# Performance work log

Hardware: AMD Instinct MI355X
Metric: run time of the kernel (lower is better)

The kernel has to match this reference:

```python
import math
import jax, jax.numpy as jnp
import numpy as np

B, S, D = 2, 2048, 1024
H = 8
HD = D // H // 2            # 64, per-branch head dim
ROT = HD // 2               # 32, rotary rot_dim (RotaryEmbedding dim=head_dim//2)
DEPTH = 2
LAMBDA_INIT = 0.8 - 0.6 * math.exp(-0.3 * DEPTH)


def rope(t):
    # t: (b, s, heads, HD); rotate first ROT dims with interleaved pairs
    s = t.shape[1]
    inv = 1.0 / (10000.0 ** (jnp.arange(0, ROT, 2, dtype=jnp.float32) / ROT))  # (ROT/2,)
    freqs = jnp.arange(s, dtype=jnp.float32)[:, None] * inv                    # (s, ROT/2)
    freqs = jnp.repeat(freqs, 2, axis=-1)                                      # (s, ROT)
    cos = jnp.cos(freqs)[None, :, None, :]
    sin = jnp.sin(freqs)[None, :, None, :]
    tl, tr = t[..., :ROT], t[..., ROT:]
    xp = tl.reshape(tl.shape[:-1] + (ROT // 2, 2))
    rh = jnp.stack((-xp[..., 1], xp[..., 0]), axis=-1).reshape(tl.shape)
    return jnp.concatenate([tl * cos + rh * sin, tr], axis=-1)


def rmsnorm(x, w, b, eps=1e-8):
    return x * jax.lax.rsqrt(jnp.mean(x * x, axis=-1, keepdims=True) + eps) * w + b


def layernorm(x, w, b, eps=1e-5):
    m = jnp.mean(x, axis=-1, keepdims=True)
    v = jnp.mean((x - m) ** 2, axis=-1, keepdims=True)
    return (x - m) * jax.lax.rsqrt(v + eps) * w + b


def causal_attn(q, k, v):
    # q,k: (b,s,h,dqk)  v: (b,s,h,dv) -> (b,s,h,dv); flash default scale 1/sqrt(dqk)
    s = q.shape[1]
    scores = jnp.einsum('bqhd,bkhd->bhqk', q, k) / jnp.sqrt(jnp.asarray(q.shape[-1], q.dtype))
    mask = jnp.tril(jnp.ones((s, s), dtype=bool))
    scores = jnp.where(mask, scores, jnp.asarray(-jnp.inf, scores.dtype))
    p = jax.nn.softmax(scores, axis=-1)
    return jnp.einsum('bhqk,bkhe->bqhe', p, v)


def setup_inputs() -> dict:
    key = jax.random.key(0)
    ks = jax.random.split(key, 16)
    f32 = jnp.float32
    inp = {
        'x': jax.random.normal(ks[0], (B, S, D), dtype=f32),
        'sigmas': jax.random.normal(ks[1], (B, HD), dtype=f32),
        'w_qkv': jax.random.normal(ks[2], (D, 3 * D), dtype=f32) * 0.02,
        'w_out': jax.random.normal(ks[3], (D, D), dtype=f32) * 0.02,
        'lq1': jax.random.normal(ks[4], (HD,), dtype=f32) * 0.1,
        'lk1': jax.random.normal(ks[5], (HD,), dtype=f32) * 0.1,
        'lq2': jax.random.normal(ks[6], (HD,), dtype=f32) * 0.1,
        'lk2': jax.random.normal(ks[7], (HD,), dtype=f32) * 0.1,
        'ln_w': jnp.ones((2 * HD,), f32) + 0.02 * jax.random.normal(ks[8], (2 * HD,), dtype=f32),
        'ln_b': 0.02 * jax.random.normal(ks[9], (2 * HD,), dtype=f32),
        'lnq_w': jnp.ones((HD,), f32) + 0.02 * jax.random.normal(ks[10], (HD,), dtype=f32),
        'lnq_b': 0.02 * jax.random.normal(ks[11], (HD,), dtype=f32),
        'ln1_w': jnp.ones((D,), f32), 'ln1_b': jnp.zeros((D,), f32),
        'ln2_w': jnp.ones((D,), f32), 'ln2_b': jnp.zeros((D,), f32),
        'w1': jax.random.normal(ks[12], (D, 4 * D), dtype=f32) * 0.02,
        'b1': jnp.zeros((4 * D,), f32),
        'w2': jax.random.normal(ks[13], (4 * D, D), dtype=f32) * 0.02,
        'b2': jnp.zeros((D,), f32),
    }
    return inp


def reference(x, sigmas, w_qkv, w_out, lq1, lk1, lq2, lk2, ln_w, ln_b,
              lnq_w, lnq_b, ln1_w, ln1_b, ln2_w, ln2_b, w1, b1, w2, b2):
    b, s, d = x.shape
    qkv = x @ w_qkv
    q, k, v = jnp.split(qkv, 3, axis=-1)
    q = q.reshape(b, s, 2 * H, HD)
    k = k.reshape(b, s, 2 * H, HD)
    v = v.reshape(b, s, H, 2 * HD)
    q = rope(q)
    k = rope(k)
    q = q.reshape(b, s, H, 2, HD)
    k = k.reshape(b, s, H, 2, HD)
    q1, q2 = q[..., 0, :], q[..., 1, :]
    k1, k2 = k[..., 0, :], k[..., 1, :]
    sig = sigmas[:, None, None, :]  # (b,1,1,HD)
    attn1 = causal_attn(q1, k1, v)
    attn2 = causal_attn(rmsnorm(q2 + sig, lnq_w, lnq_b), rmsnorm(k2 + sig, lnq_w, lnq_b), v)
    lam = jnp.exp(jnp.sum(lq1 * lk1)) - jnp.exp(jnp.sum(lq2 * lk2)) + LAMBDA_INIT
    a = rmsnorm(attn1 - lam * attn2, ln_w, ln_b) * (1.0 - LAMBDA_INIT)
    a = a.reshape(b, s, d) @ w_out
    h = layernorm(a + x, ln1_w, ln1_b)
    ff = jax.nn.silu(h @ w1 + b1) @ w2 + b2
    return layernorm(ff + h, ln2_w, ln2_b)
```

## Files before the change

### kernel.cpp

```cpp
#include <hip/hip_runtime.h>
#include <math.h>
#include <stdint.h>

#define B_ 2
#define S_ 2048
#define D_ 1024
#define H_ 8
#define NT_ (B_*S_)

static constexpr float LAMBDA_INIT = 0.47071301834358415f;
static constexpr float ONE_MINUS_LI = 1.0f - 0.47071301834358415f;

typedef __attribute__((ext_vector_type(8))) short bf16x8;
typedef __attribute__((ext_vector_type(4))) float f32x4;

__device__ __forceinline__ unsigned short f2bf(float x) {
    union { float f; unsigned int u; } v; v.f = x;
    unsigned int r = v.u + 0x7fffu + ((v.u >> 16) & 1u);
    return (unsigned short)(r >> 16);
}
__device__ __forceinline__ float bf2f(unsigned short b) {
    union { unsigned int u; float f; } v; v.u = ((unsigned int)b) << 16;
    return v.f;
}

#define GLD16(gp, lp) __builtin_amdgcn_global_load_lds( \
    (const __attribute__((address_space(1))) void*)(gp), \
    (__attribute__((address_space(3))) void*)(lp), 16, 0, 0)

__global__ void lam_kernel(const float* __restrict__ lq1, const float* __restrict__ lk1,
                           const float* __restrict__ lq2, const float* __restrict__ lk2,
                           float* __restrict__ lam_out) {
    int t = threadIdx.x;
    float p1 = lq1[t] * lk1[t];
    float p2 = lq2[t] * lk2[t];
    for (int off = 32; off; off >>= 1) {
        p1 += __shfl_xor(p1, off);
        p2 += __shfl_xor(p2, off);
    }
    if (t == 0) lam_out[0] = expf(p1) - expf(p2) + LAMBDA_INIT;
}

__global__ __launch_bounds__(256) void prep_kernel(const float* __restrict__ x,
                                                   const float* __restrict__ w_qkv,
                                                   const float* __restrict__ w_out,
                                                   const float* __restrict__ w1,
                                                   const float* __restrict__ w2,
                                                   short* __restrict__ x_bf,
                                                   short* __restrict__ w_qkvT,
                                                   short* __restrict__ w_outT,
                                                   short* __restrict__ w1T,
                                                   short* __restrict__ w2T) {
    const int z = blockIdx.x;
    if (z >= 12288) {
        const size_t i = ((size_t)(z - 12288) * 256 + threadIdx.x) * 4;
        float4 v = *(const float4*)(x + i);
        *(ushort4*)(x_bf + i) = make_ushort4(f2bf(v.x), f2bf(v.y), f2bf(v.z), f2bf(v.w));
        return;
    }
    const float* W; short* WT; int K, N, zz;
    if (z < 3072)      { W = w_qkv; WT = w_qkvT; K = 1024; N = 3072; zz = z; }
    else if (z < 4096) { W = w_out; WT = w_outT; K = 1024; N = 1024; zz = z - 3072; }
    else if (z < 8192) { W = w1;    WT = w1T;    K = 1024; N = 4096; zz = z - 4096; }
    else               { W = w2;    WT = w2T;    K = 4096; N = 1024; zz = z - 8192; }
    const int nx = N >> 5;
    const int bx = zz % nx, by = zz / nx;
    __shared__ float tile[32][33];
    const int t = threadIdx.x;
    const int k0 = by * 32, n0 = bx * 32;
    const int r = t >> 3, c0 = (t & 7) * 4;
    float4 v = *(const float4*)(W + (size_t)(k0 + r) * N + n0 + c0);
    tile[r][c0 + 0] = v.x; tile[r][c0 + 1] = v.y;
    tile[r][c0 + 2] = v.z; tile[r][c0 + 3] = v.w;
    __syncthreads();
    ushort4 o = make_ushort4(f2bf(tile[c0 + 0][r]), f2bf(tile[c0 + 1][r]),
                             f2bf(tile[c0 + 2][r]), f2bf(tile[c0 + 3][r]));
    *(ushort4*)(WT + (size_t)(n0 + r) * K + k0 + c0) = o;
}

__global__ __launch_bounds__(256) void vtrans_kernel(const short* __restrict__ qkv_bf,
                                                     short* __restrict__ vt) {
    __shared__ short tile[32][34];
    const int s0 = blockIdx.x * 32, e0 = blockIdx.y * 32, bh = blockIdx.z;
    const int b = bh >> 3, h = bh & 7;
    const int t = threadIdx.x, r = t >> 3, c0 = (t & 7) * 4;
    ushort4 v = *(const ushort4*)(qkv_bf + (size_t)(b * S_ + s0 + r) * 3072 + 2048 + h * 128 + e0 + c0);
    tile[r][c0 + 0] = v.x; tile[r][c0 + 1] = v.y;
    tile[r][c0 + 2] = v.z; tile[r][c0 + 3] = v.w;
    __syncthreads();
    ushort4 o = make_ushort4((unsigned short)tile[c0 + 0][r], (unsigned short)tile[c0 + 1][r],
                             (unsigned short)tile[c0 + 2][r], (unsigned short)tile[c0 + 3][r]);
    *(ushort4*)(vt + ((size_t)bh * 128 + e0 + r) * S_ + s0 + c0) = o;
}

template <int EPI, int OUTBF, int SPLITK>
__global__ __launch_bounds__(256) void gemm_bt(const short* __restrict__ A,
                                               const short* __restrict__ BT,
                                               const float* __restrict__ bias,
                                               void* __restrict__ C0,
                                               void* __restrict__ C1,
                                               int M, int N, int Kfull, int Ksub) {
    __shared__ short As[2][128 * 32];
    __shared__ short Bs[2][128 * 32];
    const int t = threadIdx.x;
    const int w = t >> 6, l = t & 63;
    const int lr = l & 15, lg = l >> 4;

    const int GX = gridDim.x;
    const int nwg = GX * gridDim.y;
    int flat = blockIdx.y * GX + blockIdx.x;
    flat = (flat & 7) * (nwg >> 3) + (flat >> 3);
    int part = 0;
    if (SPLITK) { const int per = nwg >> 1; part = flat / per; flat = flat % per; }
    const int per_part = SPLITK ? (nwg >> 1) : nwg;
    const int GYp = per_part / GX;
    const int panel = flat / (8 * GYp);
    const int idx = flat % (8 * GYp);
    const int by = idx >> 3;
    const int bx = panel * 8 + (idx & 7);
    const int row0 = by * 128, col0 = bx * 128;
    const int wr = (w >> 1) * 64, wc = (w & 1) * 64;

    f32x4 acc[4][4];
#pragma unroll
    for (int i = 0; i < 4; ++i)
#pragma unroll
        for (int j = 0; j < 4; ++j) acc[i][j] = (f32x4){0.f, 0.f, 0.f, 0.f};

    const short* Ag = A + (size_t)part * Ksub + (size_t)(row0 + w * 32 + (l >> 2)) * Kfull + (l & 3) * 8;
    const short* Bg = BT + (size_t)part * Ksub + (size_t)(col0 + w * 32 + (l >> 2)) * Kfull + (l & 3) * 8;

#pragma unroll
    for (int j = 0; j < 2; ++j) {
        GLD16(Ag + (size_t)j * 16 * Kfull, &As[0][(w * 2 + j) * 512]);
        GLD16(Bg + (size_t)j * 16 * Kfull, &Bs[0][(w * 2 + j) * 512]);
    }
    __syncthreads();

    int cur = 0;
    for (int k0 = 0; k0 < Ksub; k0 += 32) {
        const int nk = k0 + 32;
        if (nk < Ksub) {
#pragma unroll
            for (int j = 0; j < 2; ++j) {
                GLD16(Ag + nk + (size_t)j * 16 * Kfull, &As[cur ^ 1][(w * 2 + j) * 512]);
                GLD16(Bg + nk + (size_t)j * 16 * Kfull, &Bs[cur ^ 1][(w * 2 + j) * 512]);
            }
        }
        bf16x8 af[4], bfr[4];
#pragma unroll
        for (int i = 0; i < 4; ++i)
            af[i] = *(const bf16x8*)(&As[cur][(wr + i * 16 + lr) * 32 + lg * 8]);
#pragma unroll
        for (int j = 0; j < 4; ++j)
            bfr[j] = *(const bf16x8*)(&Bs[cur][(wc + j * 16 + lr) * 32 + lg * 8]);
#pragma unroll
        for (int i = 0; i < 4; ++i)
#pragma unroll
            for (int j = 0; j < 4; ++j)
                acc[i][j] = __builtin_amdgcn_mfma_f32_16x16x32_bf16(af[i], bfr[j], acc[i][j], 0, 0, 0);
        __syncthreads();
        cur ^= 1;
    }

    void* Cout = (SPLITK && part) ? C1 : C0;
#pragma unroll
    for (int i = 0; i < 4; ++i) {
#pragma unroll
        for (int j = 0; j < 4; ++j) {
            const int col = col0 + wc + j * 16 + lr;
            float bcol = (EPI >= 1) ? bias[col] : 0.f;
#pragma unroll
            for (int r = 0; r < 4; ++r) {
                const int row = row0 + wr + i * 16 + lg * 4 + r;
                float v = acc[i][j][r];
                if (EPI >= 1) v += bcol;
                if (EPI == 2) v = v / (1.0f + expf(-v));
                if (OUTBF) ((short*)Cout)[(size_t)row * N + col] = (short)f2bf(v);
                else       ((float*)Cout)[(size_t)row * N + col] = v;
            }
        }
    }
}

__global__ __launch_bounds__(256) void rope_kernel(const short* __restrict__ qkv,
                                                   const float* __restrict__ sigmas,
                                                   const float* __restrict__ lnq_w,
                                                   const float* __restrict__ lnq_b,
                                                   short* __restrict__ q1, short* __restrict__ q2n,
                                                   short* __restrict__ k1, short* __restrict__ k2n) {
    const int tok = blockIdx.x;
    const int b = tok >> 11, s = tok & 2047;
    const int t = threadIdx.x;
    const int hh = t >> 4;
    const int d0 = (t & 15) * 4;

    const short* qrow = qkv + (size_t)tok * 3072 + hh * 64 + d0;
    ushort4 qv = *(const ushort4*)qrow;
    ushort4 kv = *(const ushort4*)(qrow + 1024);
    float q[4] = {bf2f(qv.x), bf2f(qv.y), bf2f(qv.z), bf2f(qv.w)};
    float k[4] = {bf2f(kv.x), bf2f(kv.y), bf2f(kv.z), bf2f(kv.w)};

    if (d0 < 32) {
#pragma unroll
        for (int pr = 0; pr < 2; ++pr) {
            const int i = d0 / 2 + pr;
            float freq = (float)s * powf(10000.0f, -(float)i / 16.0f);
            float sn, c;
            sincosf(freq, &sn, &c);
            float x0 = q[2 * pr], x1 = q[2 * pr + 1];
            q[2 * pr]     = x0 * c - x1 * sn;
            q[2 * pr + 1] = x1 * c + x0 * sn;
            x0 = k[2 * pr]; x1 = k[2 * pr + 1];
            k[2 * pr]     = x0 * c - x1 * sn;
            k[2 * pr + 1] = x1 * c + x0 * sn;
        }
    }

    const int h = hh >> 1, j = hh & 1;
    const size_t obase = ((size_t)(b * H_ + h) * S_ + s) * 64 + d0;
    if (j == 0) {
        *(ushort4*)&q1[obase] = make_ushort4(f2bf(q[0]), f2bf(q[1]), f2bf(q[2]), f2bf(q[3]));
        *(ushort4*)&k1[obase] = make_ushort4(f2bf(k[0]), f2bf(k[1]), f2bf(k[2]), f2bf(k[3]));
    } else {
        float ssq_q = 0.f, ssq_k = 0.f;
#pragma unroll
        for (int i = 0; i < 4; ++i) {
            const float sg = sigmas[b * 64 + d0 + i];
            q[i] += sg; k[i] += sg;
            ssq_q += q[i] * q[i];
            ssq_k += k[i] * k[i];
        }
        for (int off = 1; off < 16; off <<= 1) {
            ssq_q += __shfl_xor(ssq_q, off, 16);
            ssq_k += __shfl_xor(ssq_k, off, 16);
        }
        const float rq = rsqrtf(ssq_q / 64.0f + 1e-8f);
        const float rk = rsqrtf(ssq_k / 64.0f + 1e-8f);
        float oq[4], ok[4];
#pragma unroll
        for (int i = 0; i < 4; ++i) {
            const float w = lnq_w[d0 + i], bb = lnq_b[d0 + i];
            oq[i] = q[i] * rq * w + bb;
            ok[i] = k[i] * rk * w + bb;
        }
        *(ushort4*)&q2n[obase] = make_ushort4(f2bf(oq[0]), f2bf(oq[1]), f2bf(oq[2]), f2bf(oq[3]));
        *(ushort4*)&k2n[obase] = make_ushort4(f2bf(ok[0]), f2bf(ok[1]), f2bf(ok[2]), f2bf(ok[3]));
    }
}

__device__ __forceinline__ void sm_update(f32x4 (&s)[4], float (&m)[4], float (&lsum)[4],
                                          f32x4 (&o)[8], short* __restrict__ Pw,
                                          const bool diag, const int qr0, const int k0,
                                          const int lr, const int lg) {
    float nm[4];
#pragma unroll
    for (int r = 0; r < 4; ++r) nm[r] = m[r];
#pragma unroll
    for (int ks = 0; ks < 4; ++ks) {
#pragma unroll
        for (int r = 0; r < 4; ++r) {
            float v = s[ks][r];
            if (diag && (k0 + ks * 16 + lr > qr0 + r)) v = -INFINITY;
            else v *= 0.125f;
            s[ks][r] = v;
            nm[r] = fmaxf(nm[r], v);
        }
    }
#pragma unroll
    for (int r = 0; r < 4; ++r) {
        nm[r] = fmaxf(nm[r], __shfl_xor(nm[r], 1));
        nm[r] = fmaxf(nm[r], __shfl_xor(nm[r], 2));
        nm[r] = fmaxf(nm[r], __shfl_xor(nm[r], 4));
        nm[r] = fmaxf(nm[r], __shfl_xor(nm[r], 8));
    }
    bool grow = false;
#pragma unroll
    for (int r = 0; r < 4; ++r) grow = grow || (nm[r] > m[r] + 8.0f);
    if (__any(grow)) {
        float al[4];
#pragma unroll
        for (int r = 0; r < 4; ++r) {
            al[r] = __expf(m[r] - nm[r]);
            m[r] = nm[r];
            lsum[r] *= al[r];
        }
#pragma unroll
        for (int es = 0; es < 8; ++es) {
#pragma unroll
            for (int r = 0; r < 4; ++r) o[es][r] *= al[r];
        }
    }
    float rs[4] = {0.f, 0.f, 0.f, 0.f};
#pragma unroll
    for (int ks = 0; ks < 4; ++ks) {
#pragma unroll
        for (int r = 0; r < 4; ++r) {
            float p = __expf(s[ks][r] - m[r]);
            rs[r] += p;
            Pw[(lg * 4 + r) * 72 + ks * 16 + lr] = (short)f2bf(p);
        }
    }
#pragma unroll
    for (int r = 0; r < 4; ++r) {
        rs[r] += __shfl_xor(rs[r], 1);
        rs[r] += __shfl_xor(rs[r], 2);
        rs[r] += __shfl_xor(rs[r], 4);
        rs[r] += __shfl_xor(rs[r], 8);
        lsum[r] += rs[r];
    }
}

__global__ __launch_bounds__(256, 3) void attn_part(const short* __restrict__ q1g,
                                                    const short* __restrict__ q2g,
                                                    const short* __restrict__ k1g,
                                                    const short* __restrict__ k2g,
                                                    const short* __restrict__ vt,
                                                    short* __restrict__ pO0,
                                                    short* __restrict__ pO1,
                                                    float* __restrict__ pml) {
    __shared__ short Ks1[64 * 72];
    __shared__ short Ks2[64 * 72];
    __shared__ short Vt[128 * 72];
    __shared__ short Ps[4][16 * 72];

    const int i = blockIdx.x;
    const int xcd = i & 7;
    const int slot = i >> 3;
    const int a = slot >> 6;
    const int j = slot & 63;
    const int qt = 31 - (j >> 1);
    const int part = j & 1;
    const int bh = xcd * 2 + a;
    const int q0 = qt * 64;
    const int t = threadIdx.x, w = t >> 6, l = t & 63;
    const int lr = l & 15, lg = l >> 4;

    const size_t kbase = (size_t)bh * S_ * 64;
    const size_t vbase = (size_t)bh * 128 * S_;

    bf16x8 qa1[2], qa2[2];
    {
        const size_t rb = kbase + (size_t)(q0 + w * 16 + lr) * 64;
#pragma unroll
        for (int dh = 0; dh < 2; ++dh) {
            qa1[dh] = *(const bf16x8*)(q1g + rb + dh * 32 + lg * 8);
            qa2[dh] = *(const bf16x8*)(q2g + rb + dh * 32 + lg * 8);
        }
    }

    const int nkt = qt + 1, mid = (nkt + 1) >> 1;
    const int kt0 = part ? mid : 0, kt1 = part ? nkt : mid;

    float m1[4], m2[4], l1[4], l2[4];
#pragma unroll
    for (int r = 0; r < 4; ++r) { m1[r] = -1e30f; m2[r] = -1e30f; l1[r] = 0.f; l2[r] = 0.f; }
    f32x4 o1[8], o2[8];
#pragma unroll
    for (int es = 0; es < 8; ++es) { o1[es] = (f32x4){0.f,0.f,0.f,0.f}; o2[es] = (f32x4){0.f,0.f,0.f,0.f}; }

    short* Pw = &Ps[w][0];
    const int qr0 = q0 + w * 16 + lg * 4;
    const int wrow_lo = q0 + w * 16;

    const int sr = t >> 2, sc = (t & 3) * 16;
    const int vr = t >> 1, vc = (t & 1) * 32;

    for (int kt = kt0; kt < kt1; ++kt) {
        const int k0 = kt * 64;
        __syncthreads();
        {
            const size_t g = kbase + (size_t)(k0 + sr) * 64 + sc;
            *(bf16x8*)(Ks1 + sr * 72 + sc)     = *(const bf16x8*)(k1g + g);
            *(bf16x8*)(Ks1 + sr * 72 + sc + 8) = *(const bf16x8*)(k1g + g + 8);
            *(bf16x8*)(Ks2 + sr * 72 + sc)     = *(const bf16x8*)(k2g + g);
            *(bf16x8*)(Ks2 + sr * 72 + sc + 8) = *(const bf16x8*)(k2g + g + 8);
            const size_t gv = vbase + (size_t)vr * S_ + k0 + vc;
#pragma unroll
            for (int jj = 0; jj < 4; ++jj)
                *(bf16x8*)(Vt + vr * 72 + vc + jj * 8) = *(const bf16x8*)(vt + gv + jj * 8);
        }
        __syncthreads();

        const bool diag = (k0 + 63 > wrow_lo);

        {
            f32x4 s[4];
#pragma unroll
            for (int ks = 0; ks < 4; ++ks) s[ks] = (f32x4){0.f,0.f,0.f,0.f};
            __builtin_amdgcn_s_setprio(1);
#pragma unroll
            for (int ks = 0; ks < 4; ++ks)
#pragma unroll
                for (int dh = 0; dh < 2; ++dh) {
                    bf16x8 kf = *(const bf16x8*)(Ks1 + (ks * 16 + lr) * 72 + dh * 32 + lg * 8);
                    s[ks] = __builtin_amdgcn_mfma_f32_16x16x32_bf16(qa1[dh], kf, s[ks], 0, 0, 0);
                }
            __builtin_amdgcn_s_setprio(0);
            sm_update(s, m1, l1, o1, Pw, diag, qr0, k0, lr, lg);
            __builtin_amdgcn_s_setprio(1);
#pragma unroll
            for (int kb = 0; kb < 2; ++kb) {
                bf16x8 pf = *(const bf16x8*)(Pw + lr * 72 + kb * 32 + lg * 8);
#pragma unroll
                for (int es = 0; es < 8; ++es) {
                    bf16x8 vf = *(const bf16x8*)(Vt + (es * 16 + lr) * 72 + kb * 32 + lg * 8);
                    o1[es] = __builtin_amdgcn_mfma_f32_16x16x32_bf16(pf, vf, o1[es], 0, 0, 0);
                }
            }
            __builtin_amdgcn_s_setprio(0);
        }
        {
            f32x4 s[4];
#pragma unroll
            for (int ks = 0; ks < 4; ++ks) s[ks] = (f32x4){0.f,0.f,0.f,0.f};
            __builtin_amdgcn_s_setprio(1);
#pragma unroll
            for (int ks = 0; ks < 4; ++ks)
#pragma unroll
                for (int dh = 0; dh < 2; ++dh) {
                    bf16x8 kf = *(const bf16x8*)(Ks2 + (ks * 16 + lr) * 72 + dh * 32 + lg * 8);
                    s[ks] = __builtin_amdgcn_mfma_f32_16x16x32_bf16(qa2[dh], kf, s[ks], 0, 0, 0);
                }
            __builtin_amdgcn_s_setprio(0);
            sm_update(s, m2, l2, o2, Pw, diag, qr0, k0, lr, lg);
            __builtin_amdgcn_s_setprio(1);
#pragma unroll
            for (int kb = 0; kb < 2; ++kb) {
                bf16x8 pf = *(const bf16x8*)(Pw + lr * 72 + kb * 32 + lg * 8);
#pragma unroll
                for (int es = 0; es < 8; ++es) {
                    bf16x8 vf = *(const bf16x8*)(Vt + (es * 16 + lr) * 72 + kb * 32 + lg * 8);
                    o2[es] = __builtin_amdgcn_mfma_f32_16x16x32_bf16(pf, vf, o2[es], 0, 0, 0);
                }
            }
            __builtin_amdgcn_s_setprio(0);
        }
    }

    {
        uint32_t* pO = (uint32_t*)(part ? pO1 : pO0);
        const size_t wb = (((size_t)bh * 32 + qt) * 4 + w) * 2048;
#pragma unroll
        for (int r = 0; r < 4; ++r) {
#pragma unroll
            for (int u = 0; u < 4; ++u) {
                uint32_t v1 = (uint32_t)f2bf(o1[2 * u][r]) | ((uint32_t)f2bf(o1[2 * u + 1][r]) << 16);
                pO[wb + (size_t)((r * 2 + 0) * 4 + u) * 64 + l] = v1;
                uint32_t v2 = (uint32_t)f2bf(o2[2 * u][r]) | ((uint32_t)f2bf(o2[2 * u + 1][r]) << 16);
                pO[wb + (size_t)((r * 2 + 1) * 4 + u) * 64 + l] = v2;
            }
        }
    }
    if (lr == 0) {
#pragma unroll
        for (int r = 0; r < 4; ++r) {
            const int q = q0 + w * 16 + lg * 4 + r;
            float4 v = make_float4(m1[r], l1[r], m2[r], l2[r]);
            *(float4*)&pml[(((size_t)part * 16 + bh) * S_ + q) * 4] = v;
        }
    }
}

__global__ __launch_bounds__(256) void attn_combine(const short* __restrict__ pO0,
                                                    const short* __restrict__ pO1,
                                                    const float* __restrict__ pml,
                                                    const float* __restrict__ lamp,
                                                    const float* __restrict__ ln_w,
                                                    const float* __restrict__ ln_b,
                                                    short* __restrict__ arms) {
    const int tok = blockIdx.x;
    const int b = tok >> 11, q = tok & 2047;
    const int t = threadIdx.x;
    const int h = t >> 5, ln32 = t & 31, e0 = ln32 * 4;
    const int bh = b * H_ + h;
    const float lam = lamp[0];

    float4 mla = *(const float4*)&pml[(((size_t)0 * 16 + bh) * S_ + q) * 4];
    float4 mlb = *(const float4*)&pml[(((size_t)1 * 16 + bh) * S_ + q) * 4];

    const float m1 = fmaxf(mla.x, mlb.x);
    const float aa1 = __expf(mla.x - m1), ab1 = __expf(mlb.x - m1);
    const float il1 = 1.0f / (aa1 * mla.y + ab1 * mlb.y);
    const float m2 = fmaxf(mla.z, mlb.z);
    const float aa2 = __expf(mla.z - m2), ab2 = __expf(mlb.z - m2);
    const float il2 = 1.0f / (aa2 * mla.w + ab2 * mlb.w);

    const int qt = q >> 6, w = (q >> 4) & 3, lg = (q >> 2) & 3, r = q & 3;
    const int es = ln32 >> 2, u = es >> 1, half = es & 1;
    const int lane0 = lg * 16 + (ln32 & 3) * 4;
    const size_t wb = (((size_t)bh * 32 + qt) * 4 + w) * 2048;
    const uint32_t* P0 = (const uint32_t*)pO0;
    const uint32_t* P1 = (const uint32_t*)pO1;
    const uint4 a1  = *(const uint4*)&P0[wb + (size_t)((r * 2 + 0) * 4 + u) * 64 + lane0];
    const uint4 b1v = *(const uint4*)&P1[wb + (size_t)((r * 2 + 0) * 4 + u) * 64 + lane0];
    const uint4 a2  = *(const uint4*)&P0[wb + (size_t)((r * 2 + 1) * 4 + u) * 64 + lane0];
    const uint4 b2v = *(const uint4*)&P1[wb + (size_t)((r * 2 + 1) * 4 + u) * 64 + lane0];
    const int sh = 16 * half;

    float comb[4]; float ssq = 0.f;
    {
        const uint32_t aw1[4] = {a1.x, a1.y, a1.z, a1.w};
        const uint32_t bw1[4] = {b1v.x, b1v.y, b1v.z, b1v.w};
        const uint32_t aw2[4] = {a2.x, a2.y, a2.z, a2.w};
        const uint32_t bw2[4] = {b2v.x, b2v.y, b2v.z, b2v.w};
#pragma unroll
        for (int i = 0; i < 4; ++i) {
            const float O1 = (aa1 * bf2f((unsigned short)(aw1[i] >> sh)) +
                              ab1 * bf2f((unsigned short)(bw1[i] >> sh))) * il1;
            const float O2 = (aa2 * bf2f((unsigned short)(aw2[i] >> sh)) +
                              ab2 * bf2f((unsigned short)(bw2[i] >> sh))) * il2;
            const float c = O1 - lam * O2;
            comb[i] = c; ssq += c * c;
        }
    }
    for (int off = 1; off < 32; off <<= 1) ssq += __shfl_xor(ssq, off, 32);
    const float rms = rsqrtf(ssq / 128.0f + 1e-8f);

    ushort4 o;
    unsigned short* op = (unsigned short*)&o;
#pragma unroll
    for (int i = 0; i < 4; ++i) {
        const int e = e0 + i;
        op[i] = f2bf((comb[i] * rms * ln_w[e] + ln_b[e]) * ONE_MINUS_LI);
    }
    *(ushort4*)&arms[(size_t)tok * 1024 + h * 128 + e0] = o;
}

__global__ __launch_bounds__(256) void add_ln1_kernel(const float* __restrict__ A0,
                                                      const float* __restrict__ A1,
                                                      const float* __restrict__ X,
                                                      const float* __restrict__ w,
                                                      const float* __restrict__ bvec,
                                                      short* __restrict__ out_bf) {
    const int row = blockIdx.x;
    const int t = threadIdx.x;
    __shared__ float red[4];

    float4 a0 = *(const float4*)&A0[(size_t)row * 1024 + t * 4];
    float4 a1 = *(const float4*)&A1[(size_t)row * 1024 + t * 4];
    float4 xv = *(const float4*)&X[(size_t)row * 1024 + t * 4];
    float v[4] = {a0.x + a1.x + xv.x, a0.y + a1.y + xv.y,
                  a0.z + a1.z + xv.z, a0.w + a1.w + xv.w};

    float s = v[0] + v[1] + v[2] + v[3];
    for (int off = 1; off < 64; off <<= 1) s += __shfl_xor(s, off);
    if ((t & 63) == 0) red[t >> 6] = s;
    __syncthreads();
    const float mean = (red[0] + red[1] + red[2] + red[3]) * (1.0f / 1024.0f);

    float sq = 0.f;
#pragma unroll
    for (int i = 0; i < 4; ++i) { const float d = v[i] - mean; sq += d * d; }
    __syncthreads();
    for (int off = 1; off < 64; off <<= 1) sq += __shfl_xor(sq, off);
    if ((t & 63) == 0) red[t >> 6] = sq;
    __syncthreads();
    const float var = (red[0] + red[1] + red[2] + red[3]) * (1.0f / 1024.0f);
    const float rstd = rsqrtf(var + 1e-5f);

    ushort4 o;
    unsigned short* op = (unsigned short*)&o;
#pragma unroll
    for (int i = 0; i < 4; ++i)
        op[i] = f2bf((v[i] - mean) * rstd * w[t * 4 + i] + bvec[t * 4 + i]);
    *(ushort4*)&out_bf[(size_t)row * 1024 + t * 4] = o;
}

__global__ __launch_bounds__(256) void add_ln2_kernel(const float* __restrict__ F0,
                                                      const float* __restrict__ F1,
                                                      const float* __restrict__ bias,
                                                      const short* __restrict__ Hbf,
                                                      const float* __restrict__ w,
                                                      const float* __restrict__ bvec,
                                                      float* __restrict__ out) {
    const int row = blockIdx.x;
    const int t = threadIdx.x;
    __shared__ float red[4];

    float4 f0 = *(const float4*)&F0[(size_t)row * 1024 + t * 4];
    float4 f1 = *(const float4*)&F1[(size_t)row * 1024 + t * 4];
    float4 bv = *(const float4*)&bias[t * 4];
    ushort4 hv = *(const ushort4*)&Hbf[(size_t)row * 1024 + t * 4];
    float v[4] = {f0.x + f1.x + bv.x + bf2f(hv.x), f0.y + f1.y + bv.y + bf2f(hv.y),
                  f0.z + f1.z + bv.z + bf2f(hv.z), f0.w + f1.w + bv.w + bf2f(hv.w)};

    float s = v[0] + v[1] + v[2] + v[3];
    for (int off = 1; off < 64; off <<= 1) s += __shfl_xor(s, off);
    if ((t & 63) == 0) red[t >> 6] = s;
    __syncthreads();
    const float mean = (red[0] + red[1] + red[2] + red[3]) * (1.0f / 1024.0f);

    float sq = 0.f;
#pragma unroll
    for (int i = 0; i < 4; ++i) { const float d = v[i] - mean; sq += d * d; }
    __syncthreads();
    for (int off = 1; off < 64; off <<= 1) sq += __shfl_xor(sq, off);
    if ((t & 63) == 0) red[t >> 6] = sq;
    __syncthreads();
    const float var = (red[0] + red[1] + red[2] + red[3]) * (1.0f / 1024.0f);
    const float rstd = rsqrtf(var + 1e-5f);

    float o[4];
#pragma unroll
    for (int i = 0; i < 4; ++i)
        o[i] = (v[i] - mean) * rstd * w[t * 4 + i] + bvec[t * 4 + i];
    *(float4*)&out[(size_t)row * 1024 + t * 4] = make_float4(o[0], o[1], o[2], o[3]);
}

extern "C" void kernel_launch(void* const* d_in, const int* in_sizes, int n_in,
                              void* d_out, int out_size, void* d_ws, size_t ws_size,
                              hipStream_t stream) {
    const float* x      = (const float*)d_in[0];
    const float* sigmas = (const float*)d_in[1];
    const float* w_qkv  = (const float*)d_in[2];
    const float* w_out  = (const float*)d_in[3];
    const float* lq1    = (const float*)d_in[4];
    const float* lk1    = (const float*)d_in[5];
    const float* lq2    = (const float*)d_in[6];
    const float* lk2    = (const float*)d_in[7];
    const float* ln_w   = (const float*)d_in[8];
    const float* ln_b   = (const float*)d_in[9];
    const float* lnq_w  = (const float*)d_in[10];
    const float* lnq_b  = (const float*)d_in[11];
    const float* ln1_w  = (const float*)d_in[12];
    const float* ln1_b  = (const float*)d_in[13];
    const float* ln2_w  = (const float*)d_in[14];
    const float* ln2_b  = (const float*)d_in[15];
    const float* w1     = (const float*)d_in[16];
    const float* b1     = (const float*)d_in[17];
    const float* w2     = (const float*)d_in[18];
    const float* b2     = (const float*)d_in[19];

    char* ws = (char*)d_ws;
    short* x_bf    = (short*)(ws + 0);
    short* vt      = (short*)(ws + 0);
    short* h_bf    = (short*)(ws + 0);
    short* w_qkvT  = (short*)(ws + 8388608);
    short* w_outT  = (short*)(ws + 14680064);
    short* w1T     = (short*)(ws + 16777216);
    short* w2T     = (short*)(ws + 25165824);
    short* qkv_bf  = (short*)(ws + 33554432);
    short* pO0     = (short*)(ws + 33554432);
    float* pml     = (float*)(ws + 50331648);
    float* a_p0    = (float*)(ws + 33554432);
    short* q1      = (short*)(ws + 58720256);
    short* q2n     = (short*)(ws + 62914560);
    short* k1      = (short*)(ws + 67108864);
    short* k2n     = (short*)(ws + 71303168);
    float* a_p1    = (float*)(ws + 58720256);
    short* pO1     = (short*)(ws + 75497472);
    short* arms    = (short*)(ws + 92274688);
    short* ffh     = (short*)(ws + 33554432);
    float* ff_p0   = (float*)(ws + 67108864);
    float* ff_p1   = (float*)(ws + 83886080);
    float* lam     = (float*)(ws + 100663296);

    lam_kernel<<<1, 64, 0, stream>>>(lq1, lk1, lq2, lk2, lam);
    prep_kernel<<<16384, 256, 0, stream>>>(x, w_qkv, w_out, w1, w2,
                                           x_bf, w_qkvT, w_outT, w1T, w2T);

    gemm_bt<0, 1, 0><<<dim3(24, 32), 256, 0, stream>>>(x_bf, w_qkvT, nullptr,
                                                       qkv_bf, nullptr, NT_, 3072, 1024, 1024);

    rope_kernel<<<NT_, 256, 0, stream>>>(qkv_bf, sigmas, lnq_w, lnq_b, q1, q2n, k1, k2n);
    vtrans_kernel<<<dim3(S_ / 32, 4, 16), 256, 0, stream>>>(qkv_bf, vt);

    attn_part<<<1024, 256, 0, stream>>>(q1, q2n, k1, k2n, vt, pO0, pO1, pml);
    attn_combine<<<NT_, 256, 0, stream>>>(pO0, pO1, pml, lam, ln_w, ln_b, arms);

    gemm_bt<0, 0, 1><<<dim3(8, 64), 256, 0, stream>>>(arms, w_outT, nullptr,
                                                      a_p0, a_p1, NT_, 1024, 1024, 512);

    add_ln1_kernel<<<NT_, 256, 0, stream>>>(a_p0, a_p1, x, ln1_w, ln1_b, h_bf);

    gemm_bt<2, 1, 0><<<dim3(32, 32), 256, 0, stream>>>(h_bf, w1T, b1,
                                                       ffh, nullptr, NT_, 4096, 1024, 1024);

    gemm_bt<0, 0, 1><<<dim3(8, 64), 256, 0, stream>>>(ffh, w2T, nullptr,
                                                      ff_p0, ff_p1, NT_, 1024, 4096, 2048);

    add_ln2_kernel<<<NT_, 256, 0, stream>>>(ff_p0, ff_p1, b2, h_bf, ln2_w, ln2_b,
                                            (float*)d_out);
}
```

Baseline: 321.6 us.

## Triple-buffer GEMM LDS tiles with explicit vmcnt waits and single barrier

Moves the bf16 GEMM from a double-buffered to a triple-buffered LDS pipeline that prefetches two K-steps ahead. Instead of __syncthreads, it uses explicit s_waitcnt vmcnt counts, so only the oldest outstanding global-to-LDS loads are waited on, plus a single s_barrier per iteration. The goal is more load/compute overlap and fewer full drains per K-step. The cost is 50% more LDS per block, which may reduce occupancy, and correctness now depends on the hand-written waitcnt counts and the ordering around the barrier.

After: 323.2 us. No clear change (+0.5%).

```diff
diff --git a/kernel.cpp b/kernel.cpp
--- a/kernel.cpp
+++ b/kernel.cpp
@@ -100,8 +100,8 @@
                                                void* __restrict__ C0,
                                                void* __restrict__ C1,
                                                int M, int N, int Kfull, int Ksub) {
-    __shared__ short As[2][128 * 32];
-    __shared__ short Bs[2][128 * 32];
+    __shared__ short As[3][128 * 32];
+    __shared__ short Bs[3][128 * 32];
     const int t = threadIdx.x;
     const int w = t >> 6, l = t & 63;
     const int lr = l & 15, lg = l >> 4;
@@ -130,22 +130,32 @@
     const short* Ag = A + (size_t)part * Ksub + (size_t)(row0 + w * 32 + (l >> 2)) * Kfull + (l & 3) * 8;
     const short* Bg = BT + (size_t)part * Ksub + (size_t)(col0 + w * 32 + (l >> 2)) * Kfull + (l & 3) * 8;
 
-#pragma unroll
-    for (int j = 0; j < 2; ++j) {
-        GLD16(Ag + (size_t)j * 16 * Kfull, &As[0][(w * 2 + j) * 512]);
-        GLD16(Bg + (size_t)j * 16 * Kfull, &Bs[0][(w * 2 + j) * 512]);
-    }
-    __syncthreads();
+    const int nst = Ksub >> 5;
+
+    auto stage = [&](int T, int Bf) {
+#pragma unroll
+        for (int j = 0; j < 2; ++j) {
+            GLD16(Ag + (T << 5) + (size_t)j * 16 * Kfull, &As[Bf][(w * 2 + j) * 512]);
+            GLD16(Bg + (T << 5) + (size_t)j * 16 * Kfull, &Bs[Bf][(w * 2 + j) * 512]);
+        }
+    };
+
+    stage(0, 0);
+    stage(1, 1);
 
     int cur = 0;
-    for (int k0 = 0; k0 < Ksub; k0 += 32) {
-        const int nk = k0 + 32;
-        if (nk < Ksub) {
-#pragma unroll
-            for (int j = 0; j < 2; ++j) {
-                GLD16(Ag + nk + (size_t)j * 16 * Kfull, &As[cur ^ 1][(w * 2 + j) * 512]);
-                GLD16(Bg + nk + (size_t)j * 16 * Kfull, &Bs[cur ^ 1][(w * 2 + j) * 512]);
-            }
+    for (int k = 0; k < nst; ++k) {
+        if (k + 1 < nst) {
+            asm volatile("s_waitcnt vmcnt(4)" ::: "memory");
+        } else {
+            asm volatile("s_waitcnt vmcnt(0)" ::: "memory");
+        }
+        __builtin_amdgcn_s_barrier();
+        __builtin_amdgcn_sched_barrier(0);
+        const int nk = k + 2;
+        if (nk < nst) {
+            int nb = cur + 2; if (nb >= 3) nb -= 3;
+            stage(nk, nb);
         }
         bf16x8 af[4], bfr[4];
 #pragma unroll
@@ -159,8 +169,9 @@
 #pragma unroll
             for (int j = 0; j < 4; ++j)
                 acc[i][j] = __builtin_amdgcn_mfma_f32_16x16x32_bf16(af[i], bfr[j], acc[i][j], 0, 0, 0);
-        __syncthreads();
-        cur ^= 1;
+        __builtin_amdgcn_sched_barrier(0);
+        asm volatile("s_waitcnt lgkmcnt(0)" ::: "memory");
+        cur = (cur + 1 == 3) ? 0 : cur + 1;
     }
 
     void* Cout = (SPLITK && part) ? C1 : C0;
```
